# Performance work log

Measured on AMD Instinct MI355X. Metric: run time of the kernel, lower is better.

## Reference

```python
import jax, jax.numpy as jnp
import numpy as np
from functools import partial


def conv2d(x, w, b=None, stride=1):
    # torch Conv2d(k=3, padding=1, stride=stride), NCHW / OIHW
    y = jax.lax.conv_general_dilated(
        x, w, window_strides=(stride, stride), padding=((1, 1), (1, 1)),
        dimension_numbers=("NCHW", "OIHW", "NCHW"))
    if b is not None:
        y = y + b[None, :, None, None]
    return y


def conv_offset2d(x, ow):
    """ConvOffset2D: conv -> (B*C,H,W,2) offsets -> bilinear sample of x at grid+offset."""
    B, C, H, W = x.shape
    off = conv2d(x, ow)                      # (B, 2C, H, W), no bias
    off = off.reshape(B * C, H, W, 2)        # faithful raw reshape as in torch code
    xb = x.reshape(B * C, H, W)
    rr, cc = jnp.meshgrid(jnp.arange(H, dtype=x.dtype), jnp.arange(W, dtype=x.dtype), indexing="ij")
    r = jnp.clip(off[..., 0] + rr, 0.0, H - 1)   # row coords, clamped
    c = jnp.clip(off[..., 1] + cc, 0.0, W - 1)   # col coords, clamped
    r0 = jnp.floor(r); r1 = jnp.ceil(r)
    c0 = jnp.floor(c); c1 = jnp.ceil(c)
    bi = jnp.arange(B * C)[:, None, None]

    def gather(ri, ci):
        return xb[bi, ri.astype(jnp.int32), ci.astype(jnp.int32)]

    v_lt = gather(r0, c0)  # (floor r, floor c)
    v_rb = gather(r1, c1)  # (ceil r,  ceil c)
    v_lb = gather(r0, c1)  # (floor r, ceil c)
    v_rt = gather(r1, c0)  # (ceil r,  floor c)
    fr = r - r0
    fc = c - c0
    vt = v_lt + (v_rt - v_lt) * fr
    vb = v_lb + (v_rb - v_lb) * fr
    out = vt + (vb - vt) * fc
    return out.reshape(B, C, H, W)


def setup_inputs() -> dict:
    key = jax.random.key(0)
    ks = jax.random.split(key, 16)
    C = 32
    B, H, W = 16, 256, 256

    def conv_w(k, co, ci):
        return jax.random.normal(k, (co, ci, 3, 3), jnp.float32) * (1.0 / np.sqrt(ci * 9))

    inp = {
        "x": jax.random.normal(ks[0], (B, C, H, W), jnp.float32),
        "w1": conv_w(ks[1], C, C),       "b1": jnp.zeros((C,), jnp.float32),
        "ow1": jax.random.normal(ks[2], (2 * C, C, 3, 3), jnp.float32) * 0.01,
        "w2": conv_w(ks[3], 2 * C, C),   "b2": jnp.zeros((2 * C,), jnp.float32),
        "ow2": jax.random.normal(ks[4], (4 * C, 2 * C, 3, 3), jnp.float32) * 0.01,
        "w3": conv_w(ks[5], C, 2 * C),   "b3": jnp.zeros((C,), jnp.float32),
        "ow3": jax.random.normal(ks[6], (2 * C, C, 3, 3), jnp.float32) * 0.01,
        "w4": conv_w(ks[7], C, C),       "b4": jnp.zeros((C,), jnp.float32),
    }
    return inp


def reference(x, w1, b1, ow1, w2, b2, ow2, w3, b3, ow3, w4, b4):
    # Dropout layers are identity in eval mode.
    h = jax.nn.relu(conv2d(x, w1, b1))                 # (B, C, H, W)
    h = conv_offset2d(h, ow1)
    h = jax.nn.relu(conv2d(h, w2, b2, stride=2))       # (B, 2C, H/2, W/2)
    h = conv_offset2d(h, ow2)
    h = jax.nn.relu(conv2d(h, w3, b3, stride=2))       # (B, C, H/4, W/4)
    h = conv_offset2d(h, ow3)
    h = jax.nn.relu(conv2d(h, w4, b4, stride=2))       # (B, C, H/8, W/8)
    return jnp.mean(h, axis=(2, 3), keepdims=True)     # global avg pool -> (B, C, 1, 1)
```

## Files before the change

### kernel.cpp

```cpp
#include <hip/hip_runtime.h>

typedef short short8 __attribute__((ext_vector_type(8)));
typedef float f32x4 __attribute__((ext_vector_type(4)));

__device__ __forceinline__ unsigned short f2b(float f) {
    unsigned u = __float_as_uint(f);
    u += 0x7fffu + ((u >> 16) & 1u);
    return (unsigned short)(u >> 16);
}
__device__ __forceinline__ float b2f(unsigned short h) {
    return __uint_as_float(((unsigned)h) << 16);
}

template <int C_IN, int C_OUT, int NW, int DEFORM>
__global__ __launch_bounds__(NW * 64) void conv_s1_mfma(
    const unsigned short* __restrict__ in, const unsigned short* __restrict__ wT,
    const float* __restrict__ bias, unsigned short* __restrict__ out,
    int H, int W, int relu)
{
    constexpr int LDSTR  = C_IN + 8;
    constexpr int KSTEPS = C_IN / 32;
    constexpr int CH8    = C_IN / 8;
    constexpr int COPB   = 32 * (NW / 4);
    static_assert(!DEFORM || COPB == 64, "deform fusion expects 64 conv ch/block");
    constexpr int S_IN = 18 * 18 * LDSTR;
    static_assert(!DEFORM || S_IN >= 4 * 100 * 32, "sample buffer must fit in s_in");
    __shared__ __align__(16) unsigned short s_in[S_IN];
    __shared__ __align__(16) unsigned short s_off[DEFORM ? 16 * 16 * 64 : 8];

    const int tid   = threadIdx.x;
    const int wave  = tid >> 6;
    const int wv    = wave & 3;
    const int csub  = wave >> 2;
    const int lane  = tid & 63;
    const int mlane = lane & 15;
    const int quad  = lane >> 4;

    const int nCo  = C_OUT / COPB;
    const int b    = blockIdx.z / nCo;
    const int coB  = (blockIdx.z - b * nCo) * COPB + csub * 32;
    const int row0 = blockIdx.y * 16;
    const int col0 = blockIdx.x * 16;

    for (int idx = tid; idx < 18 * 18 * CH8; idx += NW * 64) {
        int pixel = idx / CH8;
        int ch    = (idx - pixel * CH8) * 8;
        int pr    = pixel / 18;
        int pc    = pixel - pr * 18;
        int gr = row0 - 1 + pr, gc = col0 - 1 + pc;
        ulonglong2 v; v.x = 0; v.y = 0;
        if ((unsigned)gr < (unsigned)H && (unsigned)gc < (unsigned)W)
            v = *(const ulonglong2*)&in[((b * H + gr) * W + gc) * C_IN + ch];
        *(ulonglong2*)&s_in[pixel * LDSTR + ch] = v;
    }
    __syncthreads();

    f32x4 acc[2][4];
    #pragma unroll
    for (int mt = 0; mt < 2; ++mt)
        #pragma unroll
        for (int t = 0; t < 4; ++t) acc[mt][t] = (f32x4)(0.f);

    #pragma unroll 1
    for (int kk = 0; kk < KSTEPS; ++kk) {
        short8 A[2][9];
        #pragma unroll
        for (int mt = 0; mt < 2; ++mt)
            #pragma unroll
            for (int tap = 0; tap < 9; ++tap)
                A[mt][tap] = *(const short8*)&wT[(tap * C_OUT + coB + mt * 16 + mlane) * C_IN
                                                 + kk * 32 + quad * 8];

        const unsigned short* sb =
            &s_in[(wv * 4 * 18 + mlane) * LDSTR + kk * 32 + quad * 8];
        #pragma unroll
        for (int t = 0; t < 4; ++t) {
            #pragma unroll
            for (int tap = 0; tap < 9; ++tap) {
                const int dy = tap / 3, dx = tap % 3;
                short8 Bf = *(const short8*)&sb[((t + dy) * 18 + dx) * LDSTR];
                acc[0][t] = __builtin_amdgcn_mfma_f32_16x16x32_bf16(A[0][tap], Bf, acc[0][t], 0, 0, 0);
                acc[1][t] = __builtin_amdgcn_mfma_f32_16x16x32_bf16(A[1][tap], Bf, acc[1][t], 0, 0, 0);
            }
        }
    }

    if (!DEFORM) {
        #pragma unroll
        for (int mt = 0; mt < 2; ++mt) {
            const int cb = coB + mt * 16 + quad * 4;
            float4 bv;
            if (bias) bv = *(const float4*)&bias[cb]; else { bv.x = bv.y = bv.z = bv.w = 0.f; }
            #pragma unroll
            for (int t = 0; t < 4; ++t) {
                const int row = row0 + wv * 4 + t, col = col0 + mlane;
                float o0 = acc[mt][t][0] + bv.x, o1 = acc[mt][t][1] + bv.y;
                float o2 = acc[mt][t][2] + bv.z, o3 = acc[mt][t][3] + bv.w;
                if (relu) {
                    o0 = fmaxf(o0, 0.f); o1 = fmaxf(o1, 0.f);
                    o2 = fmaxf(o2, 0.f); o3 = fmaxf(o3, 0.f);
                }
                ushort4 pk; pk.x = f2b(o0); pk.y = f2b(o1); pk.z = f2b(o2); pk.w = f2b(o3);
                *(ushort4*)&out[((b * H + row) * W + col) * C_OUT + cb] = pk;
            }
        }
    } else {
        const int zb    = blockIdx.z - b * nCo;
        const int zbase = zb * 32;
        const int Hh = H >> 1, Wh = W >> 1;
        const int r8 = blockIdx.y * 8, c8 = blockIdx.x * 8;

        __syncthreads();

        #pragma unroll
        for (int mt = 0; mt < 2; ++mt) {
            const int cb  = csub * 32 + mt * 16 + quad * 4;
            const int swc = cb ^ ((mlane & 7) << 3);
            #pragma unroll
            for (int t = 0; t < 4; ++t) {
                ushort4 pk;
                pk.x = f2b(acc[mt][t][0]); pk.y = f2b(acc[mt][t][1]);
                pk.z = f2b(acc[mt][t][2]); pk.w = f2b(acc[mt][t][3]);
                *(ushort4*)&s_off[((wv * 4 + t) * 16 + mlane) * 64 + swc] = pk;
            }
        }

        for (int idx = tid; idx < 1600; idx += NW * 64) {
            const int pixel = idx >> 2;
            const int chq   = (idx & 3) * 8;
            const int reg   = pixel / 100;
            const int rem   = pixel - reg * 100;
            const int rr_   = rem / 10;
            const int cc_   = rem - rr_ * 10;
            int gr = r8 + (reg >> 1) * Hh - 1 + rr_;
            int gc = c8 + (reg & 1)  * Wh - 1 + cc_;
            gr = gr < 0 ? 0 : (gr > H - 1 ? H - 1 : gr);
            gc = gc < 0 ? 0 : (gc > W - 1 ? W - 1 : gc);
            *(ulonglong2*)&s_in[pixel * 32 + chq] =
                *(const ulonglong2*)&in[((b * H + gr) * W + gc) * C_IN + zbase + chq];
        }
        __syncthreads();

        const int ci   = tid & 31;
        const int slot = tid >> 5;
        const unsigned short* xb = in  + (long)b * H * W * C_IN + zbase + ci;
        unsigned short*       ob = out + (long)b * H * W * C_IN + zbase + ci;
        const float Hm1 = (float)(H - 1), Wm1 = (float)(W - 1);

        #pragma unroll 4
        for (int s = 0; s < 8; ++s) {
            const int pos = slot + s * 16;
            const int rl  = pos >> 4;
            const int cl  = (pos >> 1) & 7;
            const int chf = pos & 1;
            const int lr  = rl * 2 + chf;
            const int lc  = cl * 2;
            const int bix = (lr * 16 + lc) * 64;
            const ushort2 roP = *(const ushort2*)&s_off[bix +      ((2 * ci) ^ ((lc & 7) << 3))];
            const ushort2 coP = *(const ushort2*)&s_off[bix + 64 + ((2 * ci) ^ (((lc + 1) & 7) << 3))];
            #pragma unroll
            for (int ih = 0; ih < 2; ++ih) {
                const int R0 = r8 + ih * Hh, C0 = c8 + chf * Wh;
                const int rowg = R0 + rl, cg = C0 + cl;
                const float rr = fminf(fmaxf(b2f(ih ? roP.y : roP.x) + (float)rowg, 0.f), Hm1);
                const float cc = fminf(fmaxf(b2f(ih ? coP.y : coP.x) + (float)cg,   0.f), Wm1);
                const float rf = floorf(rr), cf = floorf(cc);
                const float fr = rr - rf, fc = cc - cf;
                const int irf = (int)rf, icf = (int)cf;
                const int dr1 = (fr > 0.f) ? 1 : 0;
                const int dc1 = (fc > 0.f) ? 1 : 0;
                const int lr0 = irf - R0 + 1;
                const int lc0 = icf - C0 + 1;
                float v00, v01, v10, v11;
                if ((unsigned)lr0 <= (unsigned)(9 - dr1) &&
                    (unsigned)lc0 <= (unsigned)(9 - dc1)) {
                    const int reg = ih * 2 + chf;
                    const unsigned short* sp =
                        &s_in[(reg * 100 + lr0 * 10 + lc0) * 32 + ci];
                    v00 = b2f(sp[0]);
                    v01 = b2f(sp[dc1 * 32]);
                    v10 = b2f(sp[dr1 * 320]);
                    v11 = b2f(sp[dr1 * 320 + dc1 * 32]);
                } else {
                    const int idx00 = (irf * W + icf) * C_IN;
                    const int dr = dr1 * W * C_IN, dc = dc1 * C_IN;
                    v00 = b2f(xb[idx00]);
                    v01 = b2f(xb[idx00 + dc]);
                    v10 = b2f(xb[idx00 + dr]);
                    v11 = b2f(xb[idx00 + dr + dc]);
                }
                const float vt = v00 + (v10 - v00) * fr;
                const float vb = v01 + (v11 - v01) * fr;
                const float rs = vt + (vb - vt) * fc;
                ob[(rowg * W + cg) * C_IN] = f2b(rs);
            }
        }
    }
}

template <int C_IN, int C_OUT, int NW>
__global__ __launch_bounds__(NW * 64) void conv_s2_mfma(
    const unsigned short* __restrict__ in, const unsigned short* __restrict__ wT,
    const float* __restrict__ bias, unsigned short* __restrict__ out,
    int H_in, int W_in, int relu)
{
    constexpr int LDSTR  = C_IN + 8;
    constexpr int KSTEPS = C_IN / 32;
    constexpr int CH8    = C_IN / 8;
    constexpr int COPB   = 32 * (NW / 4);
    __shared__ unsigned short s_in[17 * 17 * LDSTR];

    const int tid   = threadIdx.x;
    const int wave  = tid >> 6;
    const int wv    = wave & 3;
    const int csub  = wave >> 2;
    const int lane  = tid & 63;
    const int mlane = lane & 15;
    const int quad  = lane >> 4;

    const int H_out = H_in >> 1, W_out = W_in >> 1;
    const int nCo   = C_OUT / COPB;
    const int b     = blockIdx.z / nCo;
    const int coB   = (blockIdx.z - b * nCo) * COPB + csub * 32;
    const int orow0 = blockIdx.y * 8, ocol0 = blockIdx.x * 8;
    const int irow0 = orow0 * 2 - 1,  icol0 = ocol0 * 2 - 1;

    for (int idx = tid; idx < 17 * 17 * CH8; idx += NW * 64) {
        int pixel = idx / CH8;
        int ch    = (idx - pixel * CH8) * 8;
        int pr    = pixel / 17;
        int pc    = pixel - pr * 17;
        int gr = irow0 + pr, gc = icol0 + pc;
        ulonglong2 v; v.x = 0; v.y = 0;
        if ((unsigned)gr < (unsigned)H_in && (unsigned)gc < (unsigned)W_in)
            v = *(const ulonglong2*)&in[((b * H_in + gr) * W_in + gc) * C_IN + ch];
        *(ulonglong2*)&s_in[pixel * LDSTR + ch] = v;
    }
    __syncthreads();

    f32x4 acc[2];
    acc[0] = (f32x4)(0.f); acc[1] = (f32x4)(0.f);

    const int plr = wv * 2 + (mlane >> 3);
    const int plc = mlane & 7;

    #pragma unroll 1
    for (int kk = 0; kk < KSTEPS; ++kk) {
        short8 A[2][9];
        #pragma unroll
        for (int mt = 0; mt < 2; ++mt)
            #pragma unroll
            for (int tap = 0; tap < 9; ++tap)
                A[mt][tap] = *(const short8*)&wT[(tap * C_OUT + coB + mt * 16 + mlane) * C_IN
                                                 + kk * 32 + quad * 8];

        const unsigned short* sb0 =
            &s_in[(plr * 2 * 17 + plc * 2) * LDSTR + kk * 32 + quad * 8];
        #pragma unroll
        for (int tap = 0; tap < 9; ++tap) {
            const int dy = tap / 3, dx = tap % 3;
            short8 Bf = *(const short8*)&sb0[(dy * 17 + dx) * LDSTR];
            acc[0] = __builtin_amdgcn_mfma_f32_16x16x32_bf16(A[0][tap], Bf, acc[0], 0, 0, 0);
            acc[1] = __builtin_amdgcn_mfma_f32_16x16x32_bf16(A[1][tap], Bf, acc[1], 0, 0, 0);
        }
    }

    const int row = orow0 + plr, col = ocol0 + plc;
    #pragma unroll
    for (int mt = 0; mt < 2; ++mt) {
        const int cb = coB + mt * 16 + quad * 4;
        float4 bv;
        if (bias) bv = *(const float4*)&bias[cb]; else { bv.x = bv.y = bv.z = bv.w = 0.f; }
        float o0 = acc[mt][0] + bv.x, o1 = acc[mt][1] + bv.y;
        float o2 = acc[mt][2] + bv.z, o3 = acc[mt][3] + bv.w;
        if (relu) {
            o0 = fmaxf(o0, 0.f); o1 = fmaxf(o1, 0.f);
            o2 = fmaxf(o2, 0.f); o3 = fmaxf(o3, 0.f);
        }
        ushort4 pk; pk.x = f2b(o0); pk.y = f2b(o1); pk.z = f2b(o2); pk.w = f2b(o3);
        *(ushort4*)&out[((b * H_out + row) * W_out + col) * C_OUT + cb] = pk;
    }
}

__global__ __launch_bounds__(256) void nchw2nhwc(
    const float* __restrict__ x, unsigned short* __restrict__ out, int HW)
{
    __shared__ float s[32][65];
    const int b = blockIdx.y, p0 = blockIdx.x * 64;
    const int tid = threadIdx.x;
    #pragma unroll
    for (int k = 0; k < 8; ++k) {
        int e = tid + k * 256, ci = e >> 6, p = e & 63;
        s[ci][p] = x[(b * 32 + ci) * HW + p0 + p];
    }
    __syncthreads();
    #pragma unroll
    for (int k = 0; k < 8; ++k) {
        int e = tid + k * 256, p = e >> 5, ci = e & 31;
        out[(b * HW + p0 + p) * 32 + ci] = f2b(s[ci][p]);
    }
}

struct WTArgs {
    const float* src[7];
    unsigned short* dst[7];
    int co[7], ci[7], n[7];
};
__global__ __launch_bounds__(256) void wtrans_all(WTArgs a)
{
    const int i = blockIdx.x * 256 + threadIdx.x;
    #pragma unroll
    for (int s = 0; s < 7; ++s) {
        if (i < a.n[s]) {
            const int ci  = i % a.ci[s];
            const int rr  = i / a.ci[s];
            const int co  = rr % a.co[s];
            const int tap = rr / a.co[s];
            a.dst[s][i] = f2b(a.src[s][(co * a.ci[s] + ci) * 9 + tap]);
        }
    }
}

__global__ __launch_bounds__(256) void avgpool_nhwc(
    const unsigned short* __restrict__ in, float* __restrict__ out)
{
    const int b = blockIdx.x, tid = threadIdx.x;
    const int ci = tid & 31, pg = tid >> 5;
    float s = 0.f;
    for (int k = 0; k < 128; ++k) {
        int p = pg * 128 + k;
        s += b2f(in[(b * 1024 + p) * 32 + ci]);
    }
    __shared__ float red[8][32];
    red[pg][ci] = s;
    __syncthreads();
    if (tid < 32) {
        float t = 0.f;
        #pragma unroll
        for (int j = 0; j < 8; ++j) t += red[j][tid];
        out[b * 32 + tid] = t * (1.f / 1024.f);
    }
}

__global__ __launch_bounds__(256) void sentinel(float* out, int n, float v)
{
    int i = blockIdx.x * 256 + threadIdx.x;
    if (i < n) out[i] = v;
}

extern "C" void kernel_launch(void* const* d_in, const int* in_sizes, int n_in,
                              void* d_out, int out_size, void* d_ws, size_t ws_size,
                              hipStream_t stream) {
    (void)in_sizes; (void)n_in; (void)out_size;
    const float* x   = (const float*)d_in[0];
    const float* w1  = (const float*)d_in[1];
    const float* b1  = (const float*)d_in[2];
    const float* ow1 = (const float*)d_in[3];
    const float* w2  = (const float*)d_in[4];
    const float* b2  = (const float*)d_in[5];
    const float* ow2 = (const float*)d_in[6];
    const float* w3  = (const float*)d_in[7];
    const float* b3  = (const float*)d_in[8];
    const float* ow3 = (const float*)d_in[9];
    const float* w4  = (const float*)d_in[10];
    const float* b4  = (const float*)d_in[11];
    float* out = (float*)d_out;
    unsigned short* wsu = (unsigned short*)d_ws;

    const size_t XB = 0;
    const size_t HA = 33554432;
    const size_t DC = 134217728;
    const size_t WB = 167772160;
    const size_t total_us = WB + 165888;
    if (ws_size < total_us * 2) {
        sentinel<<<2, 256, 0, stream>>>(out, 512, 12345.0f);
        return;
    }
    unsigned short* xb = wsu + XB;
    unsigned short* hA = wsu + HA;
    unsigned short* dC = wsu + DC;
    unsigned short* wt1  = wsu + WB;
    unsigned short* owt1 = wt1 + 9216;
    unsigned short* wt2  = owt1 + 18432;
    unsigned short* owt2 = wt2 + 18432;
    unsigned short* wt3  = owt2 + 73728;
    unsigned short* owt3 = wt3 + 18432;
    unsigned short* wt4  = owt3 + 18432;

    WTArgs wa;
    wa.src[0] = w1;  wa.dst[0] = wt1;  wa.co[0] = 32;  wa.ci[0] = 32; wa.n[0] = 9216;
    wa.src[1] = ow1; wa.dst[1] = owt1; wa.co[1] = 64;  wa.ci[1] = 32; wa.n[1] = 18432;
    wa.src[2] = w2;  wa.dst[2] = wt2;  wa.co[2] = 64;  wa.ci[2] = 32; wa.n[2] = 18432;
    wa.src[3] = ow2; wa.dst[3] = owt2; wa.co[3] = 128; wa.ci[3] = 64; wa.n[3] = 73728;
    wa.src[4] = w3;  wa.dst[4] = wt3;  wa.co[4] = 32;  wa.ci[4] = 64; wa.n[4] = 18432;
    wa.src[5] = ow3; wa.dst[5] = owt3; wa.co[5] = 64;  wa.ci[5] = 32; wa.n[5] = 18432;
    wa.src[6] = w4;  wa.dst[6] = wt4;  wa.co[6] = 32;  wa.ci[6] = 32; wa.n[6] = 9216;
    wtrans_all<<<288, 256, 0, stream>>>(wa);

    nchw2nhwc<<<dim3(1024, 16), 256, 0, stream>>>(x, xb, 65536);

    conv_s1_mfma<32, 32, 4, 0><<<dim3(16, 16, 16), 256, 0, stream>>>(xb, wt1, b1, hA, 256, 256, 1);
    conv_s1_mfma<32, 64, 8, 1><<<dim3(16, 16, 16), 512, 0, stream>>>(hA, owt1, nullptr, dC, 256, 256, 0);

    conv_s2_mfma<32, 64, 8><<<dim3(16, 16, 16), 512, 0, stream>>>(dC, wt2, b2, hA, 256, 256, 1);
    conv_s1_mfma<64, 128, 8, 1><<<dim3(8, 8, 32), 512, 0, stream>>>(hA, owt2, nullptr, dC, 128, 128, 0);

    conv_s2_mfma<64, 32, 4><<<dim3(8, 8, 16), 256, 0, stream>>>(dC, wt3, b3, hA, 128, 128, 1);
    conv_s1_mfma<32, 64, 8, 1><<<dim3(4, 4, 16), 512, 0, stream>>>(hA, owt3, nullptr, dC, 64, 64, 0);

    conv_s2_mfma<32, 32, 4><<<dim3(4, 4, 16), 256, 0, stream>>>(dC, wt4, b4, hA, 64, 64, 1);
    avgpool_nhwc<<<16, 256, 0, stream>>>(hA, out);
}
```

Baseline: 559.6 us.

## Shrink LDS footprint of fused stride-1 conv via K-chunked staging and staged offsets

The input tile is now staged in LDS one 32-channel chunk at a time inside the K loop, with row stride 36 instead of C_IN+8, so the shared buffer no longer scales with C_IN. The offset buffer for the deformable fusion is cut to a quarter by having each wave write its rows in turn over four passes, each followed by sampling of the matching output rows. Together these lower LDS per block so more blocks can be resident, at the cost of extra barriers, per-K-step global reloads, and serialized offset passes.

```diff
diff --git a/kernel.cpp b/kernel.cpp
--- a/kernel.cpp
+++ b/kernel.cpp
@@ -18,15 +18,15 @@
     const float* __restrict__ bias, unsigned short* __restrict__ out,
     int H, int W, int relu)
 {
-    constexpr int LDSTR  = C_IN + 8;
+    constexpr int LDSTR  = 36;
     constexpr int KSTEPS = C_IN / 32;
-    constexpr int CH8    = C_IN / 8;
     constexpr int COPB   = 32 * (NW / 4);
     static_assert(!DEFORM || COPB == 64, "deform fusion expects 64 conv ch/block");
-    constexpr int S_IN = 18 * 18 * LDSTR;
-    static_assert(!DEFORM || S_IN >= 4 * 100 * 32, "sample buffer must fit in s_in");
-    __shared__ __align__(16) unsigned short s_in[S_IN];
-    __shared__ __align__(16) unsigned short s_off[DEFORM ? 16 * 16 * 64 : 8];
+    constexpr int S_CONV = 18 * 18 * LDSTR;
+    constexpr int S_SMP  = DEFORM ? 4 * 100 * 32 : 0;
+    constexpr int S_A    = (S_CONV > S_SMP) ? S_CONV : S_SMP;
+    __shared__ __align__(16) unsigned short s_in[S_A];
+    __shared__ __align__(16) unsigned short s_off[DEFORM ? 4 * 16 * 64 : 8];
 
     const int tid   = threadIdx.x;
     const int wave  = tid >> 6;
@@ -42,19 +42,6 @@
     const int row0 = blockIdx.y * 16;
     const int col0 = blockIdx.x * 16;
 
-    for (int idx = tid; idx < 18 * 18 * CH8; idx += NW * 64) {
-        int pixel = idx / CH8;
-        int ch    = (idx - pixel * CH8) * 8;
-        int pr    = pixel / 18;
-        int pc    = pixel - pr * 18;
-        int gr = row0 - 1 + pr, gc = col0 - 1 + pc;
-        ulonglong2 v; v.x = 0; v.y = 0;
-        if ((unsigned)gr < (unsigned)H && (unsigned)gc < (unsigned)W)
-            v = *(const ulonglong2*)&in[((b * H + gr) * W + gc) * C_IN + ch];
-        *(ulonglong2*)&s_in[pixel * LDSTR + ch] = v;
-    }
-    __syncthreads();
-
     f32x4 acc[2][4];
     #pragma unroll
     for (int mt = 0; mt < 2; ++mt)
@@ -63,6 +50,20 @@
 
     #pragma unroll 1
     for (int kk = 0; kk < KSTEPS; ++kk) {
+        if (kk) __syncthreads();
+        for (int idx = tid; idx < 18 * 18 * 4; idx += NW * 64) {
+            int pixel = idx >> 2;
+            int ch    = (idx & 3) * 8;
+            int pr    = pixel / 18;
+            int pc    = pixel - pr * 18;
+            int gr = row0 - 1 + pr, gc = col0 - 1 + pc;
+            ulonglong2 v; v.x = 0; v.y = 0;
+            if ((unsigned)gr < (unsigned)H && (unsigned)gc < (unsigned)W)
+                v = *(const ulonglong2*)&in[((b * H + gr) * W + gc) * C_IN + kk * 32 + ch];
+            *(ulonglong2*)&s_in[pixel * LDSTR + ch] = v;
+        }
+        __syncthreads();
+
         short8 A[2][9];
         #pragma unroll
         for (int mt = 0; mt < 2; ++mt)
@@ -72,7 +73,7 @@
                                                  + kk * 32 + quad * 8];
 
         const unsigned short* sb =
-            &s_in[(wv * 4 * 18 + mlane) * LDSTR + kk * 32 + quad * 8];
+            &s_in[(wv * 4 * 18 + mlane) * LDSTR + quad * 8];
         #pragma unroll
         for (int t = 0; t < 4; ++t) {
             #pragma unroll
@@ -110,20 +111,18 @@
         const int Hh = H >> 1, Wh = W >> 1;
         const int r8 = blockIdx.y * 8, c8 = blockIdx.x * 8;
 
+        ushort4 opk[2][4];
+        #pragma unroll
+        for (int mt = 0; mt < 2; ++mt)
+            #pragma unroll
+            for (int t = 0; t < 4; ++t) {
+                opk[mt][t].x = f2b(acc[mt][t][0]);
+                opk[mt][t].y = f2b(acc[mt][t][1]);
+                opk[mt][t].z = f2b(acc[mt][t][2]);
+                opk[mt][t].w = f2b(acc[mt][t][3]);
+            }
+
         __syncthreads();
-
-        #pragma unroll
-        for (int mt = 0; mt < 2; ++mt) {
-            const int cb  = csub * 32 + mt * 16 + quad * 4;
-            const int swc = cb ^ ((mlane & 7) << 3);
-            #pragma unroll
-            for (int t = 0; t < 4; ++t) {
-                ushort4 pk;
-                pk.x = f2b(acc[mt][t][0]); pk.y = f2b(acc[mt][t][1]);
-                pk.z = f2b(acc[mt][t][2]); pk.w = f2b(acc[mt][t][3]);
-                *(ushort4*)&s_off[((wv * 4 + t) * 16 + mlane) * 64 + swc] = pk;
-            }
-        }
 
         for (int idx = tid; idx < 1600; idx += NW * 64) {
             const int pixel = idx >> 2;
@@ -139,61 +138,77 @@
             *(ulonglong2*)&s_in[pixel * 32 + chq] =
                 *(const ulonglong2*)&in[((b * H + gr) * W + gc) * C_IN + zbase + chq];
         }
-        __syncthreads();
 
         const int ci   = tid & 31;
         const int slot = tid >> 5;
+        const int cl   = slot >> 1;
+        const int chf  = slot & 1;
+        const int lc   = cl * 2;
         const unsigned short* xb = in  + (long)b * H * W * C_IN + zbase + ci;
         unsigned short*       ob = out + (long)b * H * W * C_IN + zbase + ci;
         const float Hm1 = (float)(H - 1), Wm1 = (float)(W - 1);
-
-        #pragma unroll 4
-        for (int s = 0; s < 8; ++s) {
-            const int pos = slot + s * 16;
-            const int rl  = pos >> 4;
-            const int cl  = (pos >> 1) & 7;
-            const int chf = pos & 1;
-            const int lr  = rl * 2 + chf;
-            const int lc  = cl * 2;
-            const int bix = (lr * 16 + lc) * 64;
-            const ushort2 roP = *(const ushort2*)&s_off[bix +      ((2 * ci) ^ ((lc & 7) << 3))];
-            const ushort2 coP = *(const ushort2*)&s_off[bix + 64 + ((2 * ci) ^ (((lc + 1) & 7) << 3))];
-            #pragma unroll
-            for (int ih = 0; ih < 2; ++ih) {
-                const int R0 = r8 + ih * Hh, C0 = c8 + chf * Wh;
-                const int rowg = R0 + rl, cg = C0 + cl;
-                const float rr = fminf(fmaxf(b2f(ih ? roP.y : roP.x) + (float)rowg, 0.f), Hm1);
-                const float cc = fminf(fmaxf(b2f(ih ? coP.y : coP.x) + (float)cg,   0.f), Wm1);
-                const float rf = floorf(rr), cf = floorf(cc);
-                const float fr = rr - rf, fc = cc - cf;
-                const int irf = (int)rf, icf = (int)cf;
-                const int dr1 = (fr > 0.f) ? 1 : 0;
-                const int dc1 = (fc > 0.f) ? 1 : 0;
-                const int lr0 = irf - R0 + 1;
-                const int lc0 = icf - C0 + 1;
-                float v00, v01, v10, v11;
-                if ((unsigned)lr0 <= (unsigned)(9 - dr1) &&
-                    (unsigned)lc0 <= (unsigned)(9 - dc1)) {
-                    const int reg = ih * 2 + chf;
-                    const unsigned short* sp =
-                        &s_in[(reg * 100 + lr0 * 10 + lc0) * 32 + ci];
-                    v00 = b2f(sp[0]);
-                    v01 = b2f(sp[dc1 * 32]);
-                    v10 = b2f(sp[dr1 * 320]);
-                    v11 = b2f(sp[dr1 * 320 + dc1 * 32]);
-                } else {
-                    const int idx00 = (irf * W + icf) * C_IN;
-                    const int dr = dr1 * W * C_IN, dc = dc1 * C_IN;
-                    v00 = b2f(xb[idx00]);
-                    v01 = b2f(xb[idx00 + dc]);
-                    v10 = b2f(xb[idx00 + dr]);
-                    v11 = b2f(xb[idx00 + dr + dc]);
+        const int swz0 = (2 * ci) ^ ((lc & 7) << 3);
+        const int swz1 = (2 * ci) ^ (((lc + 1) & 7) << 3);
+
+        #pragma unroll
+        for (int pass = 0; pass < 4; ++pass) {
+            if (wv == pass) {
+                #pragma unroll
+                for (int mt = 0; mt < 2; ++mt) {
+                    const int cb  = csub * 32 + mt * 16 + quad * 4;
+                    const int swc = cb ^ ((mlane & 7) << 3);
+                    #pragma unroll
+                    for (int t = 0; t < 4; ++t)
+                        *(ushort4*)&s_off[(t * 16 + mlane) * 64 + swc] = opk[mt][t];
                 }
-                const float vt = v00 + (v10 - v00) * fr;
-                const float vb = v01 + (v11 - v01) * fr;
-                const float rs = vt + (vb - vt) * fc;
-                ob[(rowg * W + cg) * C_IN] = f2b(rs);
             }
+            __syncthreads();
+
+            #pragma unroll
+            for (int s2 = 0; s2 < 2; ++s2) {
+                const int rl   = pass * 2 + s2;
+                const int lrow = s2 * 2 + chf;
+                const int bix  = (lrow * 16 + lc) * 64;
+                const ushort2 roP = *(const ushort2*)&s_off[bix +      swz0];
+                const ushort2 coP = *(const ushort2*)&s_off[bix + 64 + swz1];
+                #pragma unroll
+                for (int ih = 0; ih < 2; ++ih) {
+                    const int R0 = r8 + ih * Hh, C0 = c8 + chf * Wh;
+                    const int rowg = R0 + rl, cg = C0 + cl;
+                    const float rr = fminf(fmaxf(b2f(ih ? roP.y : roP.x) + (float)rowg, 0.f), Hm1);
+                    const float cc = fminf(fmaxf(b2f(ih ? coP.y : coP.x) + (float)cg,   0.f), Wm1);
+                    const float rf = floorf(rr), cf = floorf(cc);
+                    const float fr = rr - rf, fc = cc - cf;
+                    const int irf = (int)rf, icf = (int)cf;
+                    const int dr1 = (fr > 0.f) ? 1 : 0;
+                    const int dc1 = (fc > 0.f) ? 1 : 0;
+                    const int lr0 = irf - R0 + 1;
+                    const int lc0 = icf - C0 + 1;
+                    float v00, v01, v10, v11;
+                    if ((unsigned)lr0 <= (unsigned)(9 - dr1) &&
+                        (unsigned)lc0 <= (unsigned)(9 - dc1)) {
+                        const int reg = ih * 2 + chf;
+                        const unsigned short* sp =
+                            &s_in[(reg * 100 + lr0 * 10 + lc0) * 32 + ci];
+                        v00 = b2f(sp[0]);
+                        v01 = b2f(sp[dc1 * 32]);
+                        v10 = b2f(sp[dr1 * 320]);
+                        v11 = b2f(sp[dr1 * 320 + dc1 * 32]);
+                    } else {
+                        const int idx00 = (irf * W + icf) * C_IN;
+                        const int dr = dr1 * W * C_IN, dc = dc1 * C_IN;
+                        v00 = b2f(xb[idx00]);
+                        v01 = b2f(xb[idx00 + dc]);
+                        v10 = b2f(xb[idx00 + dr]);
+                        v11 = b2f(xb[idx00 + dr + dc]);
+                    }
+                    const float vt = v00 + (v10 - v00) * fr;
+                    const float vb = v01 + (v11 - v01) * fr;
+                    const float rs = vt + (vb - vt) * fc;
+                    ob[(rowg * W + cg) * C_IN] = f2b(rs);
+                }
+            }
+            if (pass < 3) __syncthreads();
         }
     }
 }
```

Result: slower. 610.6 us (+9.1%).
